# Performance work log

Hardware: AMD Instinct MI355X
Metric: run time of the kernel (lower is better)

Reference implementation:

```python
import math
import jax, jax.numpy as jnp
import numpy as np

B, S, HID = 1, 2048, 4096
NH, NKV, D = 32, 8, 128
THETA = 10000.0


def setup_inputs() -> dict:
    key = jax.random.key(0)
    k1, k2, k3, k4, k5 = jax.random.split(key, 5)
    hidden_states = jax.random.normal(k1, (B, S, HID), dtype=jnp.float32)
    k_cache = jax.random.normal(k2, (B, NKV, S, D), dtype=jnp.float32)
    v_cache = jax.random.normal(k3, (B, NKV, S, D), dtype=jnp.float32)
    Wq = jax.random.normal(k4, (HID, NH * D), dtype=jnp.float32) * 0.02
    Wo = jax.random.normal(k5, (NH * D, HID), dtype=jnp.float32) * 0.02
    position_ids = jnp.broadcast_to(jnp.arange(S, dtype=jnp.int32), (B, S))
    # causal mask: True = masked out (torch.where(mask, -10000, scores))
    attention_mask = jnp.broadcast_to(
        jnp.triu(jnp.ones((S, S), dtype=bool), k=1)[None, None], (B, 1, S, S)
    )
    return {
        "hidden_states": hidden_states,
        "k_cache": k_cache,
        "v_cache": v_cache,
        "Wq": Wq,
        "Wo": Wo,
        "position_ids": position_ids,
        "attention_mask": attention_mask,
    }


def _rotate_half(x):
    x1, x2 = jnp.split(x, 2, axis=-1)
    return jnp.concatenate([-x2, x1], axis=-1)


def _rope_tables(position_ids):
    # Llama rotary embedding gathered at position_ids -> [B, 1, S, D]
    inv_freq = 1.0 / (THETA ** (jnp.arange(0, D, 2, dtype=jnp.float32) / D))
    freqs = position_ids[..., None].astype(jnp.float32) * inv_freq  # [B, S, D/2]
    emb = jnp.concatenate([freqs, freqs], axis=-1)  # [B, S, D]
    return jnp.cos(emb)[:, None], jnp.sin(emb)[:, None]


def reference(hidden_states, k_cache, v_cache, Wq, Wo, position_ids, attention_mask):
    G = NH // NKV  # GQA group size
    # q projection: [B, S, HID] -> [B, NH, S, D]
    q = (hidden_states @ Wq).reshape(B, S, NH, D).transpose(0, 2, 1, 3)
    cos, sin = _rope_tables(position_ids)
    q = q * cos + _rotate_half(q) * sin
    # GQA without materializing repeat_kv: group query heads over kv heads
    qg = q.reshape(B, NKV, G, S, D)
    scores = jnp.einsum("bkgsd,bktd->bkgst", qg, k_cache) / math.sqrt(D)
    scores = scores.reshape(B, NH, S, S)
    scores = jnp.where(attention_mask, jnp.float32(-10000.0), scores)
    probs = jax.nn.softmax(scores.astype(jnp.float32), axis=-1).astype(q.dtype)
    out = jnp.einsum("bkgst,bktd->bkgsd", probs.reshape(B, NKV, G, S, S), v_cache)
    out = out.reshape(B, NH, S, D).transpose(0, 2, 1, 3).reshape(B, S, NH * D)
    return out @ Wo
```

## Files before the change

### kernel.cpp

```cpp
#include <hip/hip_runtime.h>
#include <cstdint>
#include <cstddef>

#define S_LEN 2048
#define HID 4096
#define NH 32
#define NKV 8
#define HD 128

typedef __attribute__((ext_vector_type(4))) float f32x4;
typedef __attribute__((ext_vector_type(8))) short bf16x8;

__device__ __forceinline__ unsigned short f2bf(float f) {
  union { float f; uint32_t u; } v; v.f = f;
  uint32_t r = v.u + 0x7FFFu + ((v.u >> 16) & 1u);
  return (unsigned short)(r >> 16);
}

__global__ void cvt_bf16_kernel(const float* __restrict__ in,
                                unsigned short* __restrict__ out, int n4) {
  int i = blockIdx.x * blockDim.x + threadIdx.x;
  if (i >= n4) return;
  float4 v = ((const float4*)in)[i];
  ushort4 o;
  o.x = f2bf(v.x); o.y = f2bf(v.y); o.z = f2bf(v.z); o.w = f2bf(v.w);
  ((ushort4*)out)[i] = o;
}

__global__ __launch_bounds__(256) void transpose_cvt2_kernel(
    const float* __restrict__ in0, unsigned short* __restrict__ out0,
    const float* __restrict__ in1, unsigned short* __restrict__ out1,
    int R, int C) {
  __shared__ float tile[64][65];
  const float* inb = (blockIdx.z == 0) ? in0 : in1;
  unsigned short* outb = (blockIdx.z == 0) ? out0 : out1;
  const int c0 = blockIdx.x * 64, r0 = blockIdx.y * 64;
  const int tid = threadIdx.x;
#pragma unroll
  for (int p = 0; p < 4; ++p) {
    const int ch = p * 256 + tid;
    const int r = ch >> 4, off = (ch & 15) << 2;
    *(float4*)&tile[r][off] = *(const float4*)(inb + (size_t)(r0 + r) * C + c0 + off);
  }
  __syncthreads();
#pragma unroll
  for (int p = 0; p < 2; ++p) {
    const int ch = p * 256 + tid;
    const int i = ch >> 3, j0 = (ch & 7) << 3;
    bf16x8 v;
#pragma unroll
    for (int k = 0; k < 8; ++k) v[k] = (short)f2bf(tile[j0 + k][i]);
    *(bf16x8*)(outb + (size_t)(c0 + i) * R + r0 + j0) = v;
  }
}

__global__ __launch_bounds__(256) void transpose_cvt_kernel(
    const float* __restrict__ in, unsigned short* __restrict__ out, int R, int C) {
  __shared__ float tile[64][65];
  const int b = blockIdx.z;
  const float* inb = in + (size_t)b * R * C;
  unsigned short* outb = out + (size_t)b * R * C;
  const int c0 = blockIdx.x * 64, r0 = blockIdx.y * 64;
  const int tid = threadIdx.x;
#pragma unroll
  for (int p = 0; p < 4; ++p) {
    const int ch = p * 256 + tid;
    const int r = ch >> 4, off = (ch & 15) << 2;
    *(float4*)&tile[r][off] = *(const float4*)(inb + (size_t)(r0 + r) * C + c0 + off);
  }
  __syncthreads();
#pragma unroll
  for (int p = 0; p < 2; ++p) {
    const int ch = p * 256 + tid;
    const int i = ch >> 3, j0 = (ch & 7) << 3;
    bf16x8 v;
#pragma unroll
    for (int k = 0; k < 8; ++k) v[k] = (short)f2bf(tile[j0 + k][i]);
    *(bf16x8*)(outb + (size_t)(c0 + i) * R + r0 + j0) = v;
  }
}

__global__ __launch_bounds__(256, 2) void gemm_bt_kernel(
    const unsigned short* __restrict__ A, const unsigned short* __restrict__ BT,
    float* __restrict__ C, int M, int N, int K) {
  __shared__ __align__(16) unsigned short As[128 * 64];
  __shared__ __align__(16) unsigned short Bs[128 * 64];
  const int tid = threadIdx.x;
  const int lane = tid & 63;
  const int wid = tid >> 6;
  const int wm = (wid >> 1) * 64, wn = (wid & 1) * 64;
  const int g = blockIdx.x;
  const int xcd = g & 7, local = g >> 3;
  const int m0 = (xcd * 2 + (local & 1)) * 128;
  const int n0 = (local >> 1) * 128;
  const int lr = lane & 15;
  const int quad = lane >> 4;
  const int sw = lr & 7;
  f32x4 acc[4][4] = {};
  for (int kt = 0; kt < K; kt += 64) {
    __syncthreads();
#pragma unroll
    for (int p = 0; p < 4; ++p) {
      const int c = p * 256 + tid;
      const int r = c >> 3, jsrc = (c & 7) ^ (r & 7);
      __builtin_amdgcn_global_load_lds(
          (const __attribute__((address_space(1))) void*)(A + (size_t)(m0 + r) * K + kt + jsrc * 8),
          (__attribute__((address_space(3))) void*)(As + c * 8), 16, 0, 0);
      __builtin_amdgcn_global_load_lds(
          (const __attribute__((address_space(1))) void*)(BT + (size_t)(n0 + r) * K + kt + jsrc * 8),
          (__attribute__((address_space(3))) void*)(Bs + c * 8), 16, 0, 0);
    }
    __syncthreads();
#pragma unroll
    for (int h = 0; h < 2; ++h) {
      const int pos = ((h * 4 + quad) ^ sw) << 3;
      bf16x8 a[4], b[4];
#pragma unroll
      for (int t = 0; t < 4; ++t) {
        a[t] = *(const bf16x8*)(As + (wm + t * 16 + lr) * 64 + pos);
        b[t] = *(const bf16x8*)(Bs + (wn + t * 16 + lr) * 64 + pos);
      }
#pragma unroll
      for (int mt = 0; mt < 4; ++mt)
#pragma unroll
        for (int nt = 0; nt < 4; ++nt)
          acc[mt][nt] = __builtin_amdgcn_mfma_f32_16x16x32_bf16(a[mt], b[nt], acc[mt][nt], 0, 0, 0);
    }
  }
  const int qd = quad << 2;
#pragma unroll
  for (int mt = 0; mt < 4; ++mt)
#pragma unroll
    for (int nt = 0; nt < 4; ++nt) {
      const int row = m0 + wm + mt * 16 + qd;
      const int col = n0 + wn + nt * 16 + lr;
#pragma unroll
      for (int r = 0; r < 4; ++r)
        C[(size_t)(row + r) * N + col] = acc[mt][nt][r];
    }
}

__global__ __launch_bounds__(256, 2) void gemm_rope_kernel(
    const unsigned short* __restrict__ A, const unsigned short* __restrict__ BT,
    const int* __restrict__ pos_ids, unsigned short* __restrict__ Qout) {
  __shared__ __align__(16) unsigned short As[128 * 64];
  __shared__ __align__(16) unsigned short Bs[128 * 64];
  const int tid = threadIdx.x;
  const int lane = tid & 63;
  const int wid = tid >> 6;
  const int wm = wid * 32;
  const int g = blockIdx.x;
  const int xcd = g & 7, local = g >> 3;
  const int m0 = (xcd * 2 + (local & 1)) * 128;
  const int n0 = (local >> 1) * 128;
  const int lr = lane & 15;
  const int quad = lane >> 4;
  const int sw = lr & 7;
  f32x4 acc[2][8] = {};
  for (int kt = 0; kt < HID; kt += 64) {
    __syncthreads();
#pragma unroll
    for (int p = 0; p < 4; ++p) {
      const int c = p * 256 + tid;
      const int r = c >> 3, jsrc = (c & 7) ^ (r & 7);
      __builtin_amdgcn_global_load_lds(
          (const __attribute__((address_space(1))) void*)(A + (size_t)(m0 + r) * HID + kt + jsrc * 8),
          (__attribute__((address_space(3))) void*)(As + c * 8), 16, 0, 0);
      __builtin_amdgcn_global_load_lds(
          (const __attribute__((address_space(1))) void*)(BT + (size_t)(n0 + r) * HID + kt + jsrc * 8),
          (__attribute__((address_space(3))) void*)(Bs + c * 8), 16, 0, 0);
    }
    __syncthreads();
#pragma unroll
    for (int h = 0; h < 2; ++h) {
      const int pos = ((h * 4 + quad) ^ sw) << 3;
      bf16x8 a[2], b[8];
#pragma unroll
      for (int t = 0; t < 2; ++t)
        a[t] = *(const bf16x8*)(As + (wm + t * 16 + lr) * 64 + pos);
#pragma unroll
      for (int t = 0; t < 8; ++t)
        b[t] = *(const bf16x8*)(Bs + (t * 16 + lr) * 64 + pos);
#pragma unroll
      for (int mt = 0; mt < 2; ++mt)
#pragma unroll
        for (int nt = 0; nt < 8; ++nt)
          acc[mt][nt] = __builtin_amdgcn_mfma_f32_16x16x32_bf16(a[mt], b[nt], acc[mt][nt], 0, 0, 0);
    }
  }
  const int qd = quad << 2;
  const int h = n0 >> 7;
#pragma unroll
  for (int mt = 0; mt < 2; ++mt)
#pragma unroll
    for (int r = 0; r < 4; ++r) {
      const int row = m0 + wm + mt * 16 + qd + r;
      const float pos = (float)pos_ids[row];
#pragma unroll
      for (int nt = 0; nt < 4; ++nt) {
        const int i = nt * 16 + lr;
        const float invf = __expf(-(float)(2 * i) * (9.2103403719761836f / 128.0f));
        float sn, cs;
        __sincosf(pos * invf, &sn, &cs);
        const float x1 = acc[mt][nt][r], x2 = acc[mt][nt + 4][r];
        Qout[((size_t)h * S_LEN + row) * HD + i]      = f2bf(x1 * cs - x2 * sn);
        Qout[((size_t)h * S_LEN + row) * HD + i + 64] = f2bf(x2 * cs + x1 * sn);
      }
    }
}

__global__ __launch_bounds__(256, 2) void attn_kernel(
    const unsigned short* __restrict__ Q, const unsigned short* __restrict__ Kc,
    const unsigned short* __restrict__ VT, unsigned short* __restrict__ Aout) {
  __shared__ __align__(16) unsigned short Ks[128 * 136];
  __shared__ __align__(16) unsigned short Vs[128 * 136];
  const int tid = threadIdx.x, lane = tid & 63, wid = tid >> 6;
  const int qh = blockIdx.x;
  const int qt = (blockIdx.y < 8) ? (15 - (int)blockIdx.y) : ((int)blockIdx.y - 8);
  const int kvh = qh >> 2;
  const int lr = lane & 15, quad = lane >> 4;
  const float scale = 0.08838834764831843f;
  unsigned short* Pw = Ks + wid * (32 * 136);

  bf16x8 qf[2][4];
#pragma unroll
  for (int mt = 0; mt < 2; ++mt)
#pragma unroll
    for (int kk = 0; kk < 4; ++kk)
      qf[mt][kk] = *(const bf16x8*)(Q + ((size_t)qh * S_LEN + qt * 128 + wid * 32 + mt * 16 + lr) * HD + kk * 32 + quad * 8);

  f32x4 o[2][8] = {};
  float lsum[2][4] = {};

  for (int kt = 0; kt <= qt; ++kt) {
    __syncthreads();
#pragma unroll
    for (int p = 0; p < 8; ++p) {
      const int c = p * 256 + tid;
      const int r = c >> 4, off = (c & 15) << 3;
      *(bf16x8*)(Ks + r * 136 + off) = *(const bf16x8*)(Kc + ((size_t)kvh * S_LEN + kt * 128 + r) * HD + off);
      *(bf16x8*)(Vs + r * 136 + off) = *(const bf16x8*)(VT + ((size_t)kvh * HD + r) * S_LEN + kt * 128 + off);
    }
    __syncthreads();

    f32x4 sv[2][8];
#pragma unroll
    for (int mt = 0; mt < 2; ++mt)
#pragma unroll
      for (int nt = 0; nt < 8; ++nt) {
        f32x4 s = {};
#pragma unroll
        for (int kk = 0; kk < 4; ++kk) {
          bf16x8 kf = *(const bf16x8*)(Ks + (nt * 16 + lr) * 136 + kk * 32 + quad * 8);
          s = __builtin_amdgcn_mfma_f32_16x16x32_bf16(qf[mt][kk], kf, s, 0, 0, 0);
        }
        sv[mt][nt] = s;
      }
    __syncthreads();

    const bool diag = (kt == qt);
#pragma unroll
    for (int mt = 0; mt < 2; ++mt)
#pragma unroll
      for (int r = 0; r < 4; ++r) {
        const int qrow = qt * 128 + wid * 32 + mt * 16 + quad * 4 + r;
        float ls = 0.f;
#pragma unroll
        for (int nt = 0; nt < 8; ++nt) {
          float v = sv[mt][nt][r] * scale - 16.0f;
          if (diag && (kt * 128 + nt * 16 + lr) > qrow) v = -1e30f;
          const float p = __expf(v);
          ls += p;
          Pw[(mt * 16 + quad * 4 + r) * 136 + nt * 16 + lr] = f2bf(p);
        }
        lsum[mt][r] += ls;
      }
    bf16x8 pf[2][4];
#pragma unroll
    for (int mt = 0; mt < 2; ++mt)
#pragma unroll
      for (int kk = 0; kk < 4; ++kk)
        pf[mt][kk] = *(const bf16x8*)(Pw + (mt * 16 + lr) * 136 + kk * 32 + quad * 8);
#pragma unroll
    for (int dt = 0; dt < 8; ++dt)
#pragma unroll
      for (int kk = 0; kk < 4; ++kk) {
        bf16x8 vf = *(const bf16x8*)(Vs + (dt * 16 + lr) * 136 + kk * 32 + quad * 8);
        o[0][dt] = __builtin_amdgcn_mfma_f32_16x16x32_bf16(pf[0][kk], vf, o[0][dt], 0, 0, 0);
        o[1][dt] = __builtin_amdgcn_mfma_f32_16x16x32_bf16(pf[1][kk], vf, o[1][dt], 0, 0, 0);
      }
  }

#pragma unroll
  for (int mt = 0; mt < 2; ++mt)
#pragma unroll
    for (int r = 0; r < 4; ++r) {
      float l = lsum[mt][r];
#pragma unroll
      for (int sh = 1; sh < 16; sh <<= 1) l += __shfl_xor(l, sh);
      const float inv = 1.0f / l;
      const int qrow = qt * 128 + wid * 32 + mt * 16 + quad * 4 + r;
#pragma unroll
      for (int dt = 0; dt < 8; ++dt)
        Aout[(size_t)qrow * HID + qh * HD + dt * 16 + lr] = f2bf(o[mt][dt][r] * inv);
    }
}

extern "C" void kernel_launch(void* const* d_in, const int* in_sizes, int n_in,
                              void* d_out, int out_size, void* d_ws, size_t ws_size,
                              hipStream_t stream) {
  const float* hidden  = (const float*)d_in[0];
  const float* k_cache = (const float*)d_in[1];
  const float* v_cache = (const float*)d_in[2];
  const float* Wq      = (const float*)d_in[3];
  const float* Wo      = (const float*)d_in[4];
  const int*   pos     = (const int*)d_in[5];
  float* out = (float*)d_out;

  char* ws = (char*)d_ws;
  unsigned short* hidden_bf = (unsigned short*)(ws + 0);
  unsigned short* attn_bf   = hidden_bf;
  unsigned short* WqT       = (unsigned short*)(ws + 16777216);
  unsigned short* WoT       = (unsigned short*)(ws + 50331648);
  unsigned short* k_bf      = (unsigned short*)(ws + 83886080);
  unsigned short* vT        = (unsigned short*)(ws + 88080384);
  unsigned short* q_bf      = (unsigned short*)(ws + 92274688);

  cvt_bf16_kernel<<<(S_LEN * HID / 4 + 255) / 256, 256, 0, stream>>>(hidden, hidden_bf, S_LEN * HID / 4);
  cvt_bf16_kernel<<<(NKV * S_LEN * HD / 4 + 255) / 256, 256, 0, stream>>>(k_cache, k_bf, NKV * S_LEN * HD / 4);
  transpose_cvt2_kernel<<<dim3(HID / 64, HID / 64, 2), 256, 0, stream>>>(Wq, WqT, Wo, WoT, HID, HID);
  transpose_cvt_kernel<<<dim3(HD / 64, S_LEN / 64, NKV), 256, 0, stream>>>(v_cache, vT, S_LEN, HD);

  gemm_rope_kernel<<<dim3((S_LEN / 128) * (HID / 128)), 256, 0, stream>>>(hidden_bf, WqT, pos, q_bf);
  attn_kernel<<<dim3(NH, S_LEN / 128), 256, 0, stream>>>(q_bf, k_bf, vT, attn_bf);
  gemm_bt_kernel<<<dim3((S_LEN / 128) * (HID / 128)), 256, 0, stream>>>(attn_bf, WoT, out, S_LEN, HID, HID);
}
```

Before: 439.8 us.

## Restructure attention kernel with 64-key tiles and transposed MFMA operands

Result: faster. 422.1 us (-4.0%).

```diff
diff --git a/kernel.cpp b/kernel.cpp
--- a/kernel.cpp
+++ b/kernel.cpp
@@ -212,15 +212,15 @@
 __global__ __launch_bounds__(256, 2) void attn_kernel(
     const unsigned short* __restrict__ Q, const unsigned short* __restrict__ Kc,
     const unsigned short* __restrict__ VT, unsigned short* __restrict__ Aout) {
-  __shared__ __align__(16) unsigned short Ks[128 * 136];
-  __shared__ __align__(16) unsigned short Vs[128 * 136];
+  __shared__ __align__(16) unsigned short Ks[64 * 136];
+  __shared__ __align__(16) unsigned short Vs[128 * 72];
+  __shared__ __align__(16) unsigned short Ps[128 * 72];
   const int tid = threadIdx.x, lane = tid & 63, wid = tid >> 6;
   const int qh = blockIdx.x;
   const int qt = (blockIdx.y < 8) ? (15 - (int)blockIdx.y) : ((int)blockIdx.y - 8);
   const int kvh = qh >> 2;
   const int lr = lane & 15, quad = lane >> 4;
   const float scale = 0.08838834764831843f;
-  unsigned short* Pw = Ks + wid * (32 * 136);
 
   bf16x8 qf[2][4];
 #pragma unroll
@@ -230,80 +230,90 @@
       qf[mt][kk] = *(const bf16x8*)(Q + ((size_t)qh * S_LEN + qt * 128 + wid * 32 + mt * 16 + lr) * HD + kk * 32 + quad * 8);
 
   f32x4 o[2][8] = {};
-  float lsum[2][4] = {};
-
-  for (int kt = 0; kt <= qt; ++kt) {
-    __syncthreads();
-#pragma unroll
-    for (int p = 0; p < 8; ++p) {
+  float lsum[2] = {0.f, 0.f};
+
+  const int prow0 = (wid * 32 + lr) * 72;
+  const int nkt = 2 * qt + 2;
+  for (int kt2 = 0; kt2 < nkt; ++kt2) {
+    bf16x8 kr[4], vr[4];
+#pragma unroll
+    for (int p = 0; p < 4; ++p) {
       const int c = p * 256 + tid;
-      const int r = c >> 4, off = (c & 15) << 3;
-      *(bf16x8*)(Ks + r * 136 + off) = *(const bf16x8*)(Kc + ((size_t)kvh * S_LEN + kt * 128 + r) * HD + off);
-      *(bf16x8*)(Vs + r * 136 + off) = *(const bf16x8*)(VT + ((size_t)kvh * HD + r) * S_LEN + kt * 128 + off);
-    }
-    __syncthreads();
-
-    f32x4 sv[2][8];
+      kr[p] = *(const bf16x8*)(Kc + ((size_t)kvh * S_LEN + kt2 * 64 + (c >> 4)) * HD + (c & 15) * 8);
+      vr[p] = *(const bf16x8*)(VT + ((size_t)kvh * HD + (c >> 3)) * S_LEN + kt2 * 64 + (c & 7) * 8);
+    }
+    __syncthreads();
+#pragma unroll
+    for (int p = 0; p < 4; ++p) {
+      const int c = p * 256 + tid;
+      *(bf16x8*)(Ks + (c >> 4) * 136 + (c & 15) * 8) = kr[p];
+      *(bf16x8*)(Vs + (c >> 3) * 72 + (c & 7) * 8) = vr[p];
+    }
+    __syncthreads();
+
+    const bool dtile = (kt2 >= 2 * qt);
+#pragma unroll
+    for (int nt = 0; nt < 4; ++nt) {
+      f32x4 s0 = {}, s1 = {};
+#pragma unroll
+      for (int kk = 0; kk < 4; ++kk) {
+        bf16x8 kf = *(const bf16x8*)(Ks + (nt * 16 + lr) * 136 + kk * 32 + quad * 8);
+        s0 = __builtin_amdgcn_mfma_f32_16x16x32_bf16(kf, qf[0][kk], s0, 0, 0, 0);
+        s1 = __builtin_amdgcn_mfma_f32_16x16x32_bf16(kf, qf[1][kk], s1, 0, 0, 0);
+      }
+      const int skey0 = kt2 * 64 + nt * 16 + quad * 4;
+#pragma unroll
+      for (int mt = 0; mt < 2; ++mt) {
+        const f32x4 s = mt ? s1 : s0;
+        const int qrow = qt * 128 + wid * 32 + mt * 16 + lr;
+        ushort4 pk;
+        float ls = 0.f;
+        float pv[4];
+#pragma unroll
+        for (int r = 0; r < 4; ++r) {
+          float v = s[r] * scale - 16.0f;
+          if (dtile && (skey0 + r) > qrow) v = -1e30f;
+          pv[r] = __expf(v);
+          ls += pv[r];
+        }
+        pk.x = f2bf(pv[0]); pk.y = f2bf(pv[1]); pk.z = f2bf(pv[2]); pk.w = f2bf(pv[3]);
+        lsum[mt] += ls;
+        *(ushort4*)(Ps + prow0 + mt * 16 * 72 + nt * 16 + quad * 4) = pk;
+      }
+    }
+    bf16x8 pf[2][2];
 #pragma unroll
     for (int mt = 0; mt < 2; ++mt)
 #pragma unroll
-      for (int nt = 0; nt < 8; ++nt) {
-        f32x4 s = {};
-#pragma unroll
-        for (int kk = 0; kk < 4; ++kk) {
-          bf16x8 kf = *(const bf16x8*)(Ks + (nt * 16 + lr) * 136 + kk * 32 + quad * 8);
-          s = __builtin_amdgcn_mfma_f32_16x16x32_bf16(qf[mt][kk], kf, s, 0, 0, 0);
-        }
-        sv[mt][nt] = s;
-      }
-    __syncthreads();
-
-    const bool diag = (kt == qt);
-#pragma unroll
-    for (int mt = 0; mt < 2; ++mt)
-#pragma unroll
-      for (int r = 0; r < 4; ++r) {
-        const int qrow = qt * 128 + wid * 32 + mt * 16 + quad * 4 + r;
-        float ls = 0.f;
-#pragma unroll
-        for (int nt = 0; nt < 8; ++nt) {
-          float v = sv[mt][nt][r] * scale - 16.0f;
-          if (diag && (kt * 128 + nt * 16 + lr) > qrow) v = -1e30f;
-          const float p = __expf(v);
-          ls += p;
-          Pw[(mt * 16 + quad * 4 + r) * 136 + nt * 16 + lr] = f2bf(p);
-        }
-        lsum[mt][r] += ls;
-      }
-    bf16x8 pf[2][4];
-#pragma unroll
-    for (int mt = 0; mt < 2; ++mt)
-#pragma unroll
-      for (int kk = 0; kk < 4; ++kk)
-        pf[mt][kk] = *(const bf16x8*)(Pw + (mt * 16 + lr) * 136 + kk * 32 + quad * 8);
+      for (int kk = 0; kk < 2; ++kk)
+        pf[mt][kk] = *(const bf16x8*)(Ps + prow0 + mt * 16 * 72 + kk * 32 + quad * 8);
 #pragma unroll
     for (int dt = 0; dt < 8; ++dt)
 #pragma unroll
-      for (int kk = 0; kk < 4; ++kk) {
-        bf16x8 vf = *(const bf16x8*)(Vs + (dt * 16 + lr) * 136 + kk * 32 + quad * 8);
-        o[0][dt] = __builtin_amdgcn_mfma_f32_16x16x32_bf16(pf[0][kk], vf, o[0][dt], 0, 0, 0);
-        o[1][dt] = __builtin_amdgcn_mfma_f32_16x16x32_bf16(pf[1][kk], vf, o[1][dt], 0, 0, 0);
-      }
-  }
-
-#pragma unroll
-  for (int mt = 0; mt < 2; ++mt)
-#pragma unroll
-    for (int r = 0; r < 4; ++r) {
-      float l = lsum[mt][r];
-#pragma unroll
-      for (int sh = 1; sh < 16; sh <<= 1) l += __shfl_xor(l, sh);
-      const float inv = 1.0f / l;
-      const int qrow = qt * 128 + wid * 32 + mt * 16 + quad * 4 + r;
-#pragma unroll
-      for (int dt = 0; dt < 8; ++dt)
-        Aout[(size_t)qrow * HID + qh * HD + dt * 16 + lr] = f2bf(o[mt][dt][r] * inv);
-    }
+      for (int kk = 0; kk < 2; ++kk) {
+        bf16x8 vf = *(const bf16x8*)(Vs + (dt * 16 + lr) * 72 + kk * 32 + quad * 8);
+        o[0][dt] = __builtin_amdgcn_mfma_f32_16x16x32_bf16(vf, pf[0][kk], o[0][dt], 0, 0, 0);
+        o[1][dt] = __builtin_amdgcn_mfma_f32_16x16x32_bf16(vf, pf[1][kk], o[1][dt], 0, 0, 0);
+      }
+  }
+
+#pragma unroll
+  for (int mt = 0; mt < 2; ++mt) {
+    float l = lsum[mt];
+    l += __shfl_xor(l, 16);
+    l += __shfl_xor(l, 32);
+    const float inv = 1.0f / l;
+    const int qrow = qt * 128 + wid * 32 + mt * 16 + lr;
+#pragma unroll
+    for (int dt = 0; dt < 8; ++dt) {
+      ushort4 w;
+      w.x = f2bf(o[mt][dt][0] * inv);
+      w.y = f2bf(o[mt][dt][1] * inv);
+      w.z = f2bf(o[mt][dt][2] * inv);
+      w.w = f2bf(o[mt][dt][3] * inv);
+      *(ushort4*)(Aout + (size_t)qrow * HID + qh * HD + dt * 16 + quad * 4) = w;
+    }
+  }
 }
 
 extern "C" void kernel_launch(void* const* d_in, const int* in_sizes, int n_in,
```
